# Performance work log

Hardware: AMD Instinct MI355X
Metric: run time of the kernel (lower is better)

The kernel has to match this reference:

```python
import jax, jax.numpy as jnp
import numpy as np

A = 512   # input channels
B = 32    # number of capsule types
H4 = 16   # h*h pose dims per capsule


def setup_inputs() -> dict:
    key = jax.random.key(0)
    k1, k2, k3, k4, k5 = jax.random.split(key, 5)
    # Input feature map [N, A, H, W]
    x = jax.random.normal(k1, (64, A, 32, 32), dtype=jnp.float32)
    # Fused weights: B parallel 1x1 convs concatenated along out-channel dim.
    # Pose convs: B x Conv2d(A -> 16, k=1) -> [B*16, A]; activation convs: B x Conv2d(A -> 1) -> [B, A]
    bound = 1.0 / np.sqrt(A)  # PyTorch Conv2d default init range
    W_pose = jax.random.uniform(k2, (B * H4, A), minval=-bound, maxval=bound, dtype=jnp.float32)
    b_pose = jax.random.uniform(k3, (B * H4,), minval=-bound, maxval=bound, dtype=jnp.float32)
    W_act = jax.random.uniform(k4, (B, A), minval=-bound, maxval=bound, dtype=jnp.float32)
    b_act = jax.random.uniform(k5, (B,), minval=-bound, maxval=bound, dtype=jnp.float32)
    return {"x": x, "W_pose": W_pose, "b_pose": b_pose, "W_act": W_act, "b_act": b_act}


def reference(x, W_pose, b_pose, W_act, b_act):
    # 1x1 conv == channel contraction; fuse all 2*B tiny convs into two GEMMs.
    # poses: [N, B*16, H, W]
    poses = jnp.einsum('nahw,oa->nohw', x, W_pose) + b_pose[None, :, None, None]
    # activations: sigmoid([N, B, H, W])
    activations = jax.nn.sigmoid(jnp.einsum('nahw,oa->nohw', x, W_act) + b_act[None, :, None, None])
    return poses, activations
```

## Files before the change

### kernel.cpp

```cpp
#include <hip/hip_runtime.h>
#include <hip/hip_bf16.h>


typedef __attribute__((ext_vector_type(8))) short short8;
typedef __attribute__((ext_vector_type(4))) float f32x4;

#define A_CH   512
#define HW     1024
#define N_B    64
#define O_POSE 512
#define O_ACT  32
#define O_TOT  544
#define O_PAD  576
#define TM     64
#define BK     64
#define NIT    (A_CH / BK)
#define NOF    9

__device__ __forceinline__ unsigned pk(float lo, float hi) {
    __hip_bfloat162 h = __float22bfloat162_rn(make_float2(lo, hi));
    return *reinterpret_cast<unsigned*>(&h);
}

__global__ __launch_bounds__(256) void prep_w(const float* __restrict__ Wp,
                                              const float* __restrict__ Wa,
                                              unsigned short* __restrict__ Wb) {
    const int r = blockIdx.x;
    const int c = threadIdx.x * 2;
    float2 v = make_float2(0.f, 0.f);
    if (r < O_POSE)     v = *(const float2*)(Wp + (size_t)r * A_CH + c);
    else if (r < O_TOT) v = *(const float2*)(Wa + (size_t)(r - O_POSE) * A_CH + c);
    __hip_bfloat162 h = __float22bfloat162_rn(v);
    *(unsigned*)(Wb + (size_t)r * A_CH + c) = *reinterpret_cast<unsigned*>(&h);
}

__global__ __launch_bounds__(256, 2) void caps_gemm(
    const float* __restrict__ x,
    const unsigned short* __restrict__ Wb,
    const float* __restrict__ bp,
    const float* __restrict__ ba,
    float* __restrict__ out)
{
    __shared__ __align__(16) short lds[2][TM * BK];

    const int tid = threadIdx.x;
    const int m0  = blockIdx.x * TM;
    const int n   = blockIdx.y;

    const float* xn = x + (size_t)n * A_CH * HW + m0;

    const int sm = tid & 63;
    const int sk = (tid >> 6) * 16;
    const float* sbase = xn + (size_t)sk * HW + sm;

    const int s0   = sk >> 3;
    const int wswz = sm & 7;
    const int wr0  = sm * BK + ((s0 ^ wswz) << 3);
    const int wr1  = sm * BK + (((s0 + 1) ^ wswz) << 3);

    float xr[16];
    auto load_x = [&](int it) {
#pragma unroll
        for (int j = 0; j < 16; ++j)
            xr[j] = sbase[(size_t)(it * BK + j) * HW];
    };
    auto store_x = [&](int buf) {
        short8 v0, v1;
#pragma unroll
        for (int j = 0; j < 4; ++j) {
            ((unsigned*)&v0)[j] = pk(xr[2 * j],     xr[2 * j + 1]);
            ((unsigned*)&v1)[j] = pk(xr[8 + 2 * j], xr[9 + 2 * j]);
        }
        *(short8*)&lds[buf][wr0] = v0;
        *(short8*)&lds[buf][wr1] = v1;
    };

    const int lane = tid & 63;
    const int w    = tid >> 6;
    const int l16  = lane & 15;
    const int g    = lane >> 4;

    const unsigned short* wlane = Wb + (size_t)(w * 144 + l16) * A_CH + g * 8;

    int bidx[4];
#pragma unroll
    for (int fm = 0; fm < 4; ++fm) bidx[fm] = (fm * 16 + l16) * BK;
    const int bswz = l16 & 7;

    f32x4 acc[NOF][4] = {};

    load_x(0);
    store_x(0);
    __syncthreads();

    for (int it = 0; it < NIT; ++it) {
        const int cur = it & 1;
        if (it + 1 < NIT) load_x(it + 1);
#pragma unroll
        for (int ks = 0; ks < 2; ++ks) {
            short8 bF[4];
#pragma unroll
            for (int fm = 0; fm < 4; ++fm)
                bF[fm] = *(const short8*)&lds[cur][bidx[fm] + (((ks * 4 + g) ^ bswz) << 3)];
#pragma unroll
            for (int of = 0; of < NOF; ++of) {
                short8 aF = *(const short8*)(wlane + (size_t)of * 16 * A_CH + it * BK + ks * 32);
#pragma unroll
                for (int fm = 0; fm < 4; ++fm)
                    acc[of][fm] = __builtin_amdgcn_mfma_f32_16x16x32_bf16(
                        aF, bF[fm], acc[of][fm], 0, 0, 0);
            }
        }
        if (it + 1 < NIT) store_x(cur ^ 1);
        __syncthreads();
    }

    float* actOut = out + (size_t)N_B * O_POSE * HW;
    const size_t poseN = (size_t)n * O_POSE * HW;
    const size_t actN  = (size_t)n * O_ACT * HW;
    const int ob = w * 144;
#pragma unroll
    for (int of = 0; of < NOF; ++of) {
#pragma unroll
        for (int i = 0; i < 4; ++i) {
            const int R = ob + of * 16 + g * 4 + i;
            if (R >= O_TOT) continue;
            if (R < O_POSE) {
                const float bias = bp[R];
#pragma unroll
                for (int fm = 0; fm < 4; ++fm) {
                    const int cc = m0 + fm * 16 + l16;
                    __builtin_nontemporal_store(acc[of][fm][i] + bias,
                                                &out[poseN + (size_t)R * HW + cc]);
                }
            } else {
                const float bias = ba[R - O_POSE];
#pragma unroll
                for (int fm = 0; fm < 4; ++fm) {
                    const int cc = m0 + fm * 16 + l16;
                    const float v = acc[of][fm][i] + bias;
                    __builtin_nontemporal_store(1.0f / (1.0f + __expf(-v)),
                                                &actOut[actN + (size_t)(R - O_POSE) * HW + cc]);
                }
            }
        }
    }
}

extern "C" void kernel_launch(void* const* d_in, const int* in_sizes, int n_in,
                              void* d_out, int out_size, void* d_ws, size_t ws_size,
                              hipStream_t stream) {
    (void)in_sizes; (void)n_in; (void)out_size; (void)ws_size;
    const float* x  = (const float*)d_in[0];
    const float* Wp = (const float*)d_in[1];
    const float* bp = (const float*)d_in[2];
    const float* Wa = (const float*)d_in[3];
    const float* ba = (const float*)d_in[4];
    unsigned short* Wb = (unsigned short*)d_ws;

    prep_w<<<dim3(O_PAD), dim3(256), 0, stream>>>(Wp, Wa, Wb);
    caps_gemm<<<dim3(HW / TM, N_B), dim3(256), 0, stream>>>(x, Wb, bp, ba, (float*)d_out);
}
```

Measured before the change: 296.7 us.

## Halve spatial tile, raise occupancy, and prefetch x two iterations ahead

Cuts the per-block spatial tile from 64 to 32 columns, which halves the accumulators and doubles the grid. Launch bounds now request 4 blocks per SM instead of 2. The x staging becomes a two-deep register ring, so global loads are issued two K-steps ahead of their LDS store. The aim is more latency hiding through occupancy and deeper prefetch. The cost is that each block reuses the weight fragments over half as many columns, so weight traffic per output doubles.

After: 359.0 us. 21.0% more time.

```diff
diff --git a/kernel.cpp b/kernel.cpp
--- a/kernel.cpp
+++ b/kernel.cpp
@@ -12,7 +12,7 @@
 #define O_ACT  32
 #define O_TOT  544
 #define O_PAD  576
-#define TM     64
+#define TM     32
 #define BK     64
 #define NIT    (A_CH / BK)
 #define NOF    9
@@ -34,7 +34,7 @@
     *(unsigned*)(Wb + (size_t)r * A_CH + c) = *reinterpret_cast<unsigned*>(&h);
 }
 
-__global__ __launch_bounds__(256, 2) void caps_gemm(
+__global__ __launch_bounds__(256, 4) void caps_gemm(
     const float* __restrict__ x,
     const unsigned short* __restrict__ Wb,
     const float* __restrict__ bp,
@@ -49,30 +49,23 @@
 
     const float* xn = x + (size_t)n * A_CH * HW + m0;
 
-    const int sm = tid & 63;
-    const int sk = (tid >> 6) * 16;
-    const float* sbase = xn + (size_t)sk * HW + sm;
+    const int sm = tid & 31;
+    const int sg = tid >> 5;
+    const float* sbase = xn + (size_t)sg * 8 * HW + sm;
+    const int wr = sm * BK + ((sg ^ (sm & 7)) << 3);
 
-    const int s0   = sk >> 3;
-    const int wswz = sm & 7;
-    const int wr0  = sm * BK + ((s0 ^ wswz) << 3);
-    const int wr1  = sm * BK + (((s0 + 1) ^ wswz) << 3);
-
-    float xr[16];
-    auto load_x = [&](int it) {
+    float xr[2][8];
+    auto load_x = [&](int it, int bank) {
 #pragma unroll
-        for (int j = 0; j < 16; ++j)
-            xr[j] = sbase[(size_t)(it * BK + j) * HW];
+        for (int j = 0; j < 8; ++j)
+            xr[bank][j] = sbase[(size_t)(it * BK + j) * HW];
     };
-    auto store_x = [&](int buf) {
-        short8 v0, v1;
+    auto store_x = [&](int bank, int buf) {
+        short8 v;
 #pragma unroll
-        for (int j = 0; j < 4; ++j) {
-            ((unsigned*)&v0)[j] = pk(xr[2 * j],     xr[2 * j + 1]);
-            ((unsigned*)&v1)[j] = pk(xr[8 + 2 * j], xr[9 + 2 * j]);
-        }
-        *(short8*)&lds[buf][wr0] = v0;
-        *(short8*)&lds[buf][wr1] = v1;
+        for (int j = 0; j < 4; ++j)
+            ((unsigned*)&v)[j] = pk(xr[bank][2 * j], xr[bank][2 * j + 1]);
+        *(short8*)&lds[buf][wr] = v;
     };
 
     const int lane = tid & 63;
@@ -81,37 +74,36 @@
     const int g    = lane >> 4;
 
     const unsigned short* wlane = Wb + (size_t)(w * 144 + l16) * A_CH + g * 8;
-
-    int bidx[4];
-#pragma unroll
-    for (int fm = 0; fm < 4; ++fm) bidx[fm] = (fm * 16 + l16) * BK;
     const int bswz = l16 & 7;
 
-    f32x4 acc[NOF][4] = {};
+    f32x4 acc[NOF][2] = {};
 
-    load_x(0);
-    store_x(0);
+    load_x(0, 0);
+    load_x(1, 1);
+    store_x(0, 0);
     __syncthreads();
 
     for (int it = 0; it < NIT; ++it) {
         const int cur = it & 1;
-        if (it + 1 < NIT) load_x(it + 1);
+        if (it + 2 < NIT) load_x(it + 2, it & 1);
 #pragma unroll
         for (int ks = 0; ks < 2; ++ks) {
-            short8 bF[4];
+            short8 bF[2];
 #pragma unroll
-            for (int fm = 0; fm < 4; ++fm)
-                bF[fm] = *(const short8*)&lds[cur][bidx[fm] + (((ks * 4 + g) ^ bswz) << 3)];
+            for (int fm = 0; fm < 2; ++fm)
+                bF[fm] = *(const short8*)&lds[cur][(fm * 16 + l16) * BK +
+                                                   (((ks * 4 + g) ^ bswz) << 3)];
 #pragma unroll
             for (int of = 0; of < NOF; ++of) {
-                short8 aF = *(const short8*)(wlane + (size_t)of * 16 * A_CH + it * BK + ks * 32);
+                short8 aF = *(const short8*)(wlane + (size_t)of * 16 * A_CH +
+                                             it * BK + ks * 32);
 #pragma unroll
-                for (int fm = 0; fm < 4; ++fm)
+                for (int fm = 0; fm < 2; ++fm)
                     acc[of][fm] = __builtin_amdgcn_mfma_f32_16x16x32_bf16(
                         aF, bF[fm], acc[of][fm], 0, 0, 0);
             }
         }
-        if (it + 1 < NIT) store_x(cur ^ 1);
+        if (it + 1 < NIT) store_x((it + 1) & 1, cur ^ 1);
         __syncthreads();
     }
 
@@ -128,7 +120,7 @@
             if (R < O_POSE) {
                 const float bias = bp[R];
 #pragma unroll
-                for (int fm = 0; fm < 4; ++fm) {
+                for (int fm = 0; fm < 2; ++fm) {
                     const int cc = m0 + fm * 16 + l16;
                     __builtin_nontemporal_store(acc[of][fm][i] + bias,
                                                 &out[poseN + (size_t)R * HW + cc]);
@@ -136,7 +128,7 @@
             } else {
                 const float bias = ba[R - O_POSE];
 #pragma unroll
-                for (int fm = 0; fm < 4; ++fm) {
+                for (int fm = 0; fm < 2; ++fm) {
                     const int cc = m0 + fm * 16 + l16;
                     const float v = acc[of][fm][i] + bias;
                     __builtin_nontemporal_store(1.0f / (1.0f + __expf(-v)),
```
